# Kernel optimization log

Measured on AMD Instinct MI355X. Metric: run time of the kernel, lower is better.

Reference implementation:

```python
import jax, jax.numpy as jnp
import numpy as np
import math

C = 8  # sparsity factor c from __init__


def setup_inputs() -> dict:
    key = jax.random.key(0)
    kq, kk, kv, ki = jax.random.split(key, 4)
    B, Q, KV, D = 4, 2048, 2048, 512
    U = int(Q * math.log(KV))  # 15615 sampled keys, matches torch _sampler
    q = jax.random.normal(kq, (B, Q, D), dtype=jnp.float32)
    k = jax.random.normal(kk, (B, KV, D), dtype=jnp.float32)
    v = jax.random.normal(kv, (B, KV, D), dtype=jnp.float32)
    sample_idx = jax.random.randint(ki, (B, U), 0, KV)  # per-batch random key sample
    return {"q": q, "k": k, "v": v, "sample_idx": sample_idx}


def reference(q, k, v, sample_idx):
    B, Q, D = q.shape
    KV = k.shape[1]
    u = int(C * math.log(Q))  # number of selected queries (== 60 here)

    # _sampler: gather sampled keys per batch -> (B, U, D)
    k_bar = jnp.take_along_axis(k, sample_idx[:, :, None], axis=1)

    # sparsity measure M = max_j s_bar - mean_j s_bar, s_bar: (B, Q, U)
    s_bar = jnp.einsum('bqd,bud->bqu', q, k_bar)
    M = s_bar.max(axis=2) - s_bar.mean(axis=2)  # (B, Q)

    # top-u queries per batch
    _, top_idx = jax.lax.top_k(M, u)  # (B, u)
    q_bar = jnp.take_along_axis(q, top_idx[:, :, None], axis=1)  # (B, u, D)

    # small dense attention over full keys; NOTE: original scales by sqrt(kv_len)
    attn = jnp.einsum('bud,bkd->buk', q_bar, k) / jnp.sqrt(jnp.asarray(KV, q.dtype))
    attn = jax.nn.softmax(attn, axis=-1)
    s1 = jnp.einsum('buk,bkd->bud', attn, v)  # (B, u, D)

    # fill all positions with mean of v, then scatter attention outputs
    s = jnp.broadcast_to(v.mean(axis=1, keepdims=True), q.shape)  # (B, Q, D)
    bidx = jnp.arange(B)[:, None]
    s = s.at[bidx, top_idx].set(s1)
    return s
```

## Files before the change

### kernel.cpp

```cpp
#include <hip/hip_runtime.h>
#include <math.h>

#define BATCH 4
#define QN    2048
#define KVN   2048
#define DN    512
#define U_TOT 15615
#define NSEL  60
#define NSLOT 32
#define S1KS  64

typedef __attribute__((ext_vector_type(8))) short bf16x8;
typedef __attribute__((ext_vector_type(4))) float f32x4;

__device__ __forceinline__ unsigned short f2bf(float f) {
  unsigned u = __float_as_uint(f);
  unsigned r = (u + 0x7fffu + ((u >> 16) & 1u)) >> 16;
  return (unsigned short)r;
}
__device__ __forceinline__ float bf2f(unsigned short h) {
  return __uint_as_float(((unsigned)h) << 16);
}
__device__ __forceinline__ void gld16(const void* g, void* l) {
  __builtin_amdgcn_global_load_lds(
      (const __attribute__((address_space(1))) unsigned int*)g,
      (__attribute__((address_space(3))) unsigned int*)l, 16, 0, 0);
}

__global__ __launch_bounds__(256) void split_kernel(
    const float* __restrict__ q, const float* __restrict__ k,
    unsigned short* __restrict__ qhi, unsigned short* __restrict__ qlo,
    unsigned short* __restrict__ khi, unsigned short* __restrict__ klo)
{
  const int half = blockIdx.x >> 12;
  const int i = (blockIdx.x & 4095) * 256 + threadIdx.x;
  const float* in = half ? k : q;
  unsigned short* hi = half ? khi : qhi;
  unsigned short* lo = half ? klo : qlo;
  float4 f = reinterpret_cast<const float4*>(in)[i];
  ushort4 h, l;
  h.x = f2bf(f.x); l.x = f2bf(f.x - bf2f(h.x));
  h.y = f2bf(f.y); l.y = f2bf(f.y - bf2f(h.y));
  h.z = f2bf(f.z); l.z = f2bf(f.z - bf2f(h.z));
  h.w = f2bf(f.w); l.w = f2bf(f.w - bf2f(h.w));
  reinterpret_cast<ushort4*>(hi)[i] = h;
  reinterpret_cast<ushort4*>(lo)[i] = l;
}

__global__ __launch_bounds__(1024) void count_kernel(
    const int* __restrict__ sidx, float* __restrict__ cnt)
{
  __shared__ int h[KVN];
  const int b = blockIdx.x, t = threadIdx.x;
  for (int i = t; i < KVN; i += 1024) h[i] = 0;
  __syncthreads();
  for (int i = t; i < U_TOT; i += 1024) atomicAdd(&h[sidx[b * U_TOT + i]], 1);
  __syncthreads();
  for (int i = t; i < KVN; i += 1024) cnt[b * KVN + i] = (float)h[i];
}

#define BAR() asm volatile("s_barrier" ::: "memory")

#define PHASE_MFMA(P) \
  __builtin_amdgcn_s_setprio(1); \
  _Pragma("unroll") \
  for (int n = 0; n < 4; ++n) { \
    acc[2*(P)][n]   = __builtin_amdgcn_mfma_f32_16x16x32_bf16(a0h, bh_[n], acc[2*(P)][n], 0, 0, 0); \
    acc[2*(P)][n]   = __builtin_amdgcn_mfma_f32_16x16x32_bf16(a0h, bl_[n], acc[2*(P)][n], 0, 0, 0); \
    acc[2*(P)][n]   = __builtin_amdgcn_mfma_f32_16x16x32_bf16(a0l, bh_[n], acc[2*(P)][n], 0, 0, 0); \
    acc[2*(P)+1][n] = __builtin_amdgcn_mfma_f32_16x16x32_bf16(a1h, bh_[n], acc[2*(P)+1][n], 0, 0, 0); \
    acc[2*(P)+1][n] = __builtin_amdgcn_mfma_f32_16x16x32_bf16(a1h, bl_[n], acc[2*(P)+1][n], 0, 0, 0); \
    acc[2*(P)+1][n] = __builtin_amdgcn_mfma_f32_16x16x32_bf16(a1l, bh_[n], acc[2*(P)+1][n], 0, 0, 0); \
  } \
  __builtin_amdgcn_s_setprio(0);

#define LOAD_A(P, CB) \
  a0h = *reinterpret_cast<const bf16x8*>(&Ah[CB][(4*(P)+wr)*512 + fr8]); \
  a0l = *reinterpret_cast<const bf16x8*>(&Al[CB][(4*(P)+wr)*512 + fr8]); \
  a1h = *reinterpret_cast<const bf16x8*>(&Ah[CB][(4*(P)+2+wr)*512 + fr8]); \
  a1l = *reinterpret_cast<const bf16x8*>(&Al[CB][(4*(P)+2+wr)*512 + fr8]);

#define LOAD_B(CB) \
  _Pragma("unroll") \
  for (int n = 0; n < 4; ++n) { \
    bh_[n] = *reinterpret_cast<const bf16x8*>(&Bh[CB][wc*2048 + n*512 + fr8]); \
    bl_[n] = *reinterpret_cast<const bf16x8*>(&Bl[CB][wc*2048 + n*512 + fr8]); \
  }

#define KSTEP_MAIN(CB, NB) { \
  gld16(kh0, &Bh[NB][t*8]); gld16(kh1, &Bh[NB][4096 + t*8]); \
  gld16(kl0, &Bl[NB][t*8]); gld16(kl1, &Bl[NB][4096 + t*8]); \
  gld16(qh0, &Ah[NB][t*8]); gld16(ql0, &Al[NB][t*8]); \
  gld16(qh1, &Ah[NB][4096 + t*8]); gld16(ql1, &Al[NB][4096 + t*8]); \
  kh0 += 32; kh1 += 32; kl0 += 32; kl1 += 32; \
  qh0 += 32; qh1 += 32; ql0 += 32; ql1 += 32; \
  { \
    bf16x8 bh_[4], bl_[4], a0h, a0l, a1h, a1l; \
    LOAD_B(CB) \
    LOAD_A(0, CB) \
    PHASE_MFMA(0) \
    LOAD_A(1, CB) \
    PHASE_MFMA(1) \
    LOAD_A(2, CB) \
    PHASE_MFMA(2) \
    LOAD_A(3, CB) \
    PHASE_MFMA(3) \
  } \
  asm volatile("s_waitcnt vmcnt(0)" ::: "memory"); \
  BAR(); \
}

#define KSTEP_LAST(CB) { \
  bf16x8 bh_[4], bl_[4], a0h, a0l, a1h, a1l; \
  LOAD_B(CB) \
  LOAD_A(0, CB) \
  PHASE_MFMA(0) \
  LOAD_A(1, CB) \
  PHASE_MFMA(1) \
  LOAD_A(2, CB) \
  PHASE_MFMA(2) \
  LOAD_A(3, CB) \
  PHASE_MFMA(3) \
}

__global__ __launch_bounds__(512, 2) void s_mfma_kernel(
    const unsigned short* __restrict__ qh, const unsigned short* __restrict__ ql,
    const unsigned short* __restrict__ kh, const unsigned short* __restrict__ kl,
    const float* __restrict__ cnt, float* __restrict__ Pmax, float* __restrict__ Psum)
{
  __shared__ __align__(16) unsigned short Ah[2][8192];
  __shared__ __align__(16) unsigned short Al[2][8192];
  __shared__ __align__(16) unsigned short Bh[2][8192];
  __shared__ __align__(16) unsigned short Bl[2][8192];
  __shared__ float cnt_s[256];

  const int t = threadIdx.x;
  const int w = t >> 6;
  const int L = t & 63;
  const int lm = L & 15;
  const int wr = w >> 2;
  const int wc = w & 3;

  const int bid = blockIdx.x;
  const int xcd = bid & 7;
  const int idx = bid >> 3;
  const int b   = xcd >> 1;
  const int ji  = (xcd & 1) * 4 + (idx >> 3);
  const int qi  = idx & 7;
  const int j0  = ji * 256;
  const int q0  = qi * 256;

  if (t < 256) cnt_s[t] = cnt[b * KVN + j0 + t];

  const int srow = t >> 2;
  const int schk = (t & 3) ^ ((t >> 3) & 3);
  const int perm = (L >> 4) ^ ((lm >> 1) & 3);
  const int fr8  = (4 * lm + perm) * 8;

  const size_t kof = ((size_t)(b * KVN) + j0 + srow) * DN + (size_t)(schk * 8);
  const size_t qof = ((size_t)(b * QN) + q0 + srow) * DN + (size_t)(schk * 8);
  const unsigned short* kh0 = kh + kof;
  const unsigned short* kh1 = kh0 + (size_t)128 * DN;
  const unsigned short* kl0 = kl + kof;
  const unsigned short* kl1 = kl0 + (size_t)128 * DN;
  const unsigned short* qh0 = qh + qof;
  const unsigned short* qh1 = qh0 + (size_t)128 * DN;
  const unsigned short* ql0 = ql + qof;
  const unsigned short* ql1 = ql0 + (size_t)128 * DN;

  f32x4 acc[8][4];
#pragma unroll
  for (int m = 0; m < 8; ++m)
#pragma unroll
    for (int n = 0; n < 4; ++n) {
      acc[m][n][0] = 0.f; acc[m][n][1] = 0.f;
      acc[m][n][2] = 0.f; acc[m][n][3] = 0.f;
    }

  gld16(kh0, &Bh[0][t*8]); gld16(kh1, &Bh[0][4096 + t*8]);
  gld16(kl0, &Bl[0][t*8]); gld16(kl1, &Bl[0][4096 + t*8]);
  gld16(qh0, &Ah[0][t*8]); gld16(ql0, &Al[0][t*8]);
  gld16(qh1, &Ah[0][4096 + t*8]); gld16(ql1, &Al[0][4096 + t*8]);
  kh0 += 32; kh1 += 32; kl0 += 32; kl1 += 32;
  qh0 += 32; qh1 += 32; ql0 += 32; ql1 += 32;
  asm volatile("s_waitcnt vmcnt(0) lgkmcnt(0)" ::: "memory");
  BAR();

#pragma unroll 1
  for (int it = 0; it < 7; ++it) {
    KSTEP_MAIN(0, 1)
    KSTEP_MAIN(1, 0)
  }
  KSTEP_MAIN(0, 1)
  KSTEP_LAST(1)

  const int slot = ji * 4 + wc;
  const size_t spi = (size_t)(slot * BATCH + b);
  const int rgrp = (L >> 4) * 4;
#pragma unroll
  for (int m = 0; m < 8; ++m) {
    float mx[4] = {-INFINITY, -INFINITY, -INFINITY, -INFINITY};
    float ws[4] = {0.f, 0.f, 0.f, 0.f};
#pragma unroll
    for (int n = 0; n < 4; ++n) {
      const float cw = cnt_s[wc * 64 + n * 16 + lm];
      const bool has = (cw > 0.f);
#pragma unroll
      for (int r = 0; r < 4; ++r) {
        const float v = acc[m][n][r];
        if (has) mx[r] = fmaxf(mx[r], v);
        ws[r] = fmaf(cw, v, ws[r]);
      }
    }
#pragma unroll
    for (int r = 0; r < 4; ++r) {
      float mval = mx[r], sval = ws[r];
#pragma unroll
      for (int o = 1; o < 16; o <<= 1) {
        mval = fmaxf(mval, __shfl_xor(mval, o));
        sval += __shfl_xor(sval, o);
      }
      if (lm == 0) {
        const int qrow = q0 + (2 * m + wr) * 16 + rgrp + r;
        Pmax[spi * QN + qrow] = mval;
        Psum[spi * QN + qrow] = sval;
      }
    }
  }
}

__global__ __launch_bounds__(256) void combine_kernel(
    const float* __restrict__ Pmax, const float* __restrict__ Psum, float* __restrict__ M)
{
  const int g = blockIdx.x * 256 + threadIdx.x;
  const int b = g >> 11;
  const int qq = g & (QN - 1);
  float m = -INFINITY, s = 0.f;
#pragma unroll 4
  for (int p = 0; p < NSLOT; ++p) {
    m = fmaxf(m, Pmax[((size_t)(p * BATCH + b)) * QN + qq]);
    s += Psum[((size_t)(p * BATCH + b)) * QN + qq];
  }
  M[g] = m - s * (1.0f / (float)U_TOT);
}

__global__ __launch_bounds__(256) void select_kernel(
    const float* __restrict__ M, int* __restrict__ topidx, int* __restrict__ rowslot)
{
  const int b = blockIdx.x;
  const int t = threadIdx.x;
  unsigned long long key[8];
#pragma unroll
  for (int s = 0; s < 8; ++s) {
    const int qq = s * 256 + t;
    unsigned u = __float_as_uint(M[b * QN + qq]);
    u = (u & 0x80000000u) ? ~u : (u | 0x80000000u);
    key[s] = ((unsigned long long)u << 32) | (unsigned)(QN - qq);
    rowslot[b * QN + qq] = -1;
  }

  __shared__ unsigned hist[256];
  __shared__ unsigned long long pref_s;
  __shared__ unsigned rank_s;
  __shared__ unsigned cnt_s;
  if (t == 0) { pref_s = 0ull; rank_s = NSEL; cnt_s = 0u; }
  __syncthreads();

  for (int level = 7; level >= 0; --level) {
    const int shift = level * 8;
    hist[t] = 0;
    __syncthreads();
    const unsigned long long pref = pref_s;
    const unsigned rank = rank_s;
#pragma unroll
    for (int s = 0; s < 8; ++s) {
      const bool match = (level == 7) || ((key[s] >> (shift + 8)) == pref);
      if (match) atomicAdd(&hist[(unsigned)((key[s] >> shift) & 255u)], 1u);
    }
    __syncthreads();
    if (t < 64) {
      const unsigned h0 = hist[4 * t], h1 = hist[4 * t + 1];
      const unsigned h2 = hist[4 * t + 2], h3 = hist[4 * t + 3];
      const unsigned loc = h0 + h1 + h2 + h3;
      unsigned run = loc;
#pragma unroll
      for (int o = 1; o < 64; o <<= 1) {
        const unsigned oth = (unsigned)__shfl_down((int)run, o);
        if (t + o < 64) run += oth;
      }
      const unsigned suf = run - loc;
      const unsigned c3 = suf, c2 = c3 + h3, c1 = c2 + h2, c0 = c1 + h1;
      int hit = -1; unsigned cgt = 0;
      if      (c3 < rank && rank <= c3 + h3) { hit = 4 * t + 3; cgt = c3; }
      else if (c2 < rank && rank <= c2 + h2) { hit = 4 * t + 2; cgt = c2; }
      else if (c1 < rank && rank <= c1 + h1) { hit = 4 * t + 1; cgt = c1; }
      else if (c0 < rank && rank <= c0 + h0) { hit = 4 * t + 0; cgt = c0; }
      if (hit >= 0) {
        pref_s = ((level == 7) ? 0ull : (pref_s << 8)) | (unsigned long long)(unsigned)hit;
        rank_s = rank - cgt;
      }
    }
    __syncthreads();
  }

  const unsigned long long T = pref_s;
#pragma unroll
  for (int s = 0; s < 8; ++s) {
    if (key[s] >= T) {
      const unsigned pos = atomicAdd(&cnt_s, 1u);
      const int qsel = QN - (int)(key[s] & 0xFFFFFFFFull);
      topidx[b * 64 + pos] = qsel;
      rowslot[b * QN + qsel] = (int)pos;
    }
  }
}

#define SBM 64
#define SBN 32
#define SBK 32
__global__ __launch_bounds__(256) void scores_kernel(
    const float* __restrict__ q, const int* __restrict__ topidx,
    const float* __restrict__ k, float* __restrict__ attn)
{
  __shared__ float a_s[SBK][SBM + 4];
  __shared__ float b_s[SBK][SBN + 4];
  __shared__ int tix_s[64];
  const int t  = threadIdx.x;
  const int tx = t & 7;
  const int ty = t >> 3;
  const int kv0 = blockIdx.x * SBN;
  const int b   = blockIdx.y;
  const float* kb = k + (size_t)b * KVN * DN;

  if (t < 64) tix_s[t] = (t < NSEL) ? topidx[b * 64 + t] : 0;
  __syncthreads();

  float acc[2][4];
#pragma unroll
  for (int i = 0; i < 2; ++i)
#pragma unroll
    for (int j = 0; j < 4; ++j) acc[i][j] = 0.f;

  const int c4 = (t & 7) * 4;
  const int r0 = t >> 3;
  const int srow0 = tix_s[r0];
  const int srow1 = tix_s[r0 + 32];

  for (int d0 = 0; d0 < DN; d0 += SBK) {
#pragma unroll
    for (int rr = 0; rr < 2; ++rr) {
      int row = r0 + rr * 32;
      int srow = rr ? srow1 : srow0;
      float4 av = *reinterpret_cast<const float4*>(q + ((size_t)(b * QN) + srow) * DN + d0 + c4);
      a_s[c4 + 0][row] = av.x; a_s[c4 + 1][row] = av.y;
      a_s[c4 + 2][row] = av.z; a_s[c4 + 3][row] = av.w;
    }
    {
      float4 bv = *reinterpret_cast<const float4*>(kb + (size_t)(kv0 + r0) * DN + d0 + c4);
      b_s[c4 + 0][r0] = bv.x; b_s[c4 + 1][r0] = bv.y;
      b_s[c4 + 2][r0] = bv.z; b_s[c4 + 3][r0] = bv.w;
    }
    __syncthreads();
#pragma unroll
    for (int kk = 0; kk < SBK; ++kk) {
      const float a0 = a_s[kk][ty * 2];
      const float a1 = a_s[kk][ty * 2 + 1];
      float4 bv = *reinterpret_cast<const float4*>(&b_s[kk][tx * 4]);
      float bf[4] = {bv.x, bv.y, bv.z, bv.w};
#pragma unroll
      for (int j = 0; j < 4; ++j) {
        acc[0][j] = fmaf(a0, bf[j], acc[0][j]);
        acc[1][j] = fmaf(a1, bf[j], acc[1][j]);
      }
    }
    __syncthreads();
  }

#pragma unroll
  for (int i = 0; i < 2; ++i) {
    int j = ty * 2 + i;
    if (j < NSEL) {
      float4 o = make_float4(acc[i][0], acc[i][1], acc[i][2], acc[i][3]);
      *reinterpret_cast<float4*>(attn + ((size_t)(b * NSEL + j)) * KVN + kv0 + tx * 4) = o;
    }
  }
}

__global__ __launch_bounds__(256) void softmax_kernel(float* __restrict__ attn)
{
  __shared__ float buf[KVN];
  __shared__ float red[256];
  const int t = threadIdx.x;
  float* row = attn + (size_t)blockIdx.x * KVN;

  float m = -INFINITY;
  for (int i = t; i < KVN; i += 256) { float v = row[i]; buf[i] = v; m = fmaxf(m, v); }
  red[t] = m;
  __syncthreads();
  for (int off = 128; off > 0; off >>= 1) {
    if (t < off) red[t] = fmaxf(red[t], red[t + off]);
    __syncthreads();
  }
  m = red[0];
  __syncthreads();

  const float sc = 0.022097086912079608f;
  float s = 0.f;
  for (int i = t; i < KVN; i += 256) { float e = __expf((buf[i] - m) * sc); buf[i] = e; s += e; }
  red[t] = s;
  __syncthreads();
  for (int off = 128; off > 0; off >>= 1) {
    if (t < off) red[t] += red[t + off];
    __syncthreads();
  }
  float inv = 1.f / red[0];
  for (int i = t; i < KVN; i += 256) row[i] = buf[i] * inv;
}

__global__ __launch_bounds__(256) void s1_partial_kernel(
    const float* __restrict__ attn, const float* __restrict__ v,
    float* __restrict__ part, float* __restrict__ vpart)
{
  __shared__ float a_s[32][61];
  const int t    = threadIdx.x;
  const int dv4  = t & 63;
  const int jg   = t >> 6;
  const int dh   = blockIdx.x;
  const int b    = blockIdx.y;
  const int ks   = blockIdx.z;
  const int kv0  = ks * 32;
  const int dbase = dh * 256 + dv4 * 4;

  for (int x = t; x < NSEL * 32; x += 256) {
    const int j = x >> 5, kk = x & 31;
    a_s[kk][j] = attn[((size_t)(b * NSEL + j)) * KVN + kv0 + kk];
  }
  __syncthreads();

  f32x4 acc[15];
#pragma unroll
  for (int i = 0; i < 15; ++i) { acc[i][0] = 0.f; acc[i][1] = 0.f; acc[i][2] = 0.f; acc[i][3] = 0.f; }
  f32x4 vsum; vsum[0] = 0.f; vsum[1] = 0.f; vsum[2] = 0.f; vsum[3] = 0.f;

  const float* vb = v + ((size_t)b * KVN + kv0) * DN + dbase;
#pragma unroll 8
  for (int kk = 0; kk < 32; ++kk) {
    const f32x4 vv = *reinterpret_cast<const f32x4*>(vb + (size_t)kk * DN);
    if (jg == 0) { vsum[0] += vv[0]; vsum[1] += vv[1]; vsum[2] += vv[2]; vsum[3] += vv[3]; }
#pragma unroll
    for (int jj = 0; jj < 15; ++jj) {
      const float a = a_s[kk][jg * 15 + jj];
      acc[jj][0] = fmaf(a, vv[0], acc[jj][0]);
      acc[jj][1] = fmaf(a, vv[1], acc[jj][1]);
      acc[jj][2] = fmaf(a, vv[2], acc[jj][2]);
      acc[jj][3] = fmaf(a, vv[3], acc[jj][3]);
    }
  }

#pragma unroll
  for (int jj = 0; jj < 15; ++jj) {
    const int j = jg * 15 + jj;
    *reinterpret_cast<f32x4*>(
        part + ((size_t)((ks * BATCH + b) * NSEL) + j) * DN + dbase) = acc[jj];
  }
  if (jg == 0)
    *reinterpret_cast<f32x4*>(vpart + ((size_t)(ks * BATCH + b)) * DN + dbase) = vsum;
}

__global__ void vmean_combine_kernel(const float* __restrict__ vpart, float* __restrict__ vmean)
{
  int idx = blockIdx.x * 256 + threadIdx.x;
  if (idx < BATCH * DN) {
    int b = idx / DN, d = idx % DN;
    float s = 0.f;
    for (int c = 0; c < S1KS; ++c) s += vpart[(size_t)(c * BATCH + b) * DN + d];
    vmean[idx] = s * (1.0f / (float)KVN);
  }
}

__global__ __launch_bounds__(256) void out_kernel(
    const float* __restrict__ part, const float* __restrict__ vmean,
    const int* __restrict__ rowslot, float* __restrict__ out)
{
  const int gid = blockIdx.x * 256 + threadIdx.x;
  const int d4 = gid & 127;
  const int qq = (gid >> 7) & (QN - 1);
  const int b  = gid >> 18;
  const int slot = rowslot[b * QN + qq];
  f32x4 o;
  if (slot >= 0) {
    o[0] = 0.f; o[1] = 0.f; o[2] = 0.f; o[3] = 0.f;
    for (int ks = 0; ks < S1KS; ++ks) {
      const f32x4 p = reinterpret_cast<const f32x4*>(part)[
          ((size_t)((ks * BATCH + b) * NSEL) + slot) * (DN / 4) + d4];
      o[0] += p[0]; o[1] += p[1]; o[2] += p[2]; o[3] += p[3];
    }
  } else {
    o = reinterpret_cast<const f32x4*>(vmean)[b * (DN / 4) + d4];
  }
  reinterpret_cast<f32x4*>(out)[gid] = o;
}

extern "C" void kernel_launch(void* const* d_in, const int* in_sizes, int n_in,
                              void* d_out, int out_size, void* d_ws, size_t ws_size,
                              hipStream_t stream) {
  const float* q    = (const float*)d_in[0];
  const float* k    = (const float*)d_in[1];
  const float* v    = (const float*)d_in[2];
  const int*   sidx = (const int*)d_in[3];
  float* out = (float*)d_out;
  char*  W   = (char*)d_ws;

  const size_t NEL = (size_t)BATCH * QN * DN;
  unsigned short* qh = (unsigned short*)W;
  unsigned short* ql = qh + NEL;
  unsigned short* kh = ql + NEL;
  unsigned short* kl = kh + NEL;

  char* W2 = W + 37748736;
  float* cnt     = (float*)W2;
  float* Pmax    = (float*)(W2 + 32768);
  float* Psum    = (float*)(W2 + 32768 + 1048576);
  float* Mbuf    = (float*)(W2 + 32768 + 2097152);
  int*   topidx  = (int*)(W2 + 32768 + 2097152 + 32768);
  int*   rowslot = (int*)(W2 + 32768 + 2097152 + 32768 + 4096);

  float* attn  = (float*)W;
  float* part  = (float*)(W + 2097152);
  float* vpart = (float*)(W + 33554432);
  float* vmean = (float*)(W + 34078720);

  split_kernel<<<dim3(8192), 256, 0, stream>>>(q, k, qh, ql, kh, kl);
  count_kernel<<<dim3(BATCH), 1024, 0, stream>>>(sidx, cnt);
  s_mfma_kernel<<<dim3(256), 512, 0, stream>>>(qh, ql, kh, kl, cnt, Pmax, Psum);
  combine_kernel<<<dim3(BATCH * QN / 256), 256, 0, stream>>>(Pmax, Psum, Mbuf);
  select_kernel<<<dim3(BATCH), 256, 0, stream>>>(Mbuf, topidx, rowslot);
  scores_kernel<<<dim3(KVN / SBN, BATCH), 256, 0, stream>>>(q, topidx, k, attn);
  softmax_kernel<<<dim3(BATCH * NSEL), 256, 0, stream>>>(attn);
  s1_partial_kernel<<<dim3(2, BATCH, S1KS), 256, 0, stream>>>(attn, v, part, vpart);
  vmean_combine_kernel<<<dim3(8), 256, 0, stream>>>(vpart, vmean);
  out_kernel<<<dim3(4096), 256, 0, stream>>>(part, vmean, rowslot, out);
}
```

Before: 220.8 us.

## Fuse preprocessing, combine, and softmax into neighboring kernels with deferred normalization

Merges the bf16 split, sample count histogram, and v column-sum into one launch, folds the M combine step into the top-k selection kernel, and removes the separate softmax kernel. Exp is now applied in the scores epilogue, with row sums accumulated in s1_partial and division applied in out_kernel. The s1 KV chunk doubles to halve partial sums. This cuts launch count and attn round trips, but drops max-subtraction in softmax, which risks overflow for large scores, and uses float atomics for the v mean.

Measured after the change: 238.6 us. 1.08x slower.

```diff
diff --git a/kernel.cpp b/kernel.cpp
--- a/kernel.cpp
+++ b/kernel.cpp
@@ -8,7 +8,7 @@
 #define U_TOT 15615
 #define NSEL  60
 #define NSLOT 32
-#define S1KS  64
+#define S1KS  32
 
 typedef __attribute__((ext_vector_type(8))) short bf16x8;
 typedef __attribute__((ext_vector_type(4))) float f32x4;
@@ -27,36 +27,50 @@
       (__attribute__((address_space(3))) unsigned int*)l, 16, 0, 0);
 }
 
-__global__ __launch_bounds__(256) void split_kernel(
+__global__ __launch_bounds__(256) void pre_kernel(
     const float* __restrict__ q, const float* __restrict__ k,
+    const float* __restrict__ v, const int* __restrict__ sidx,
     unsigned short* __restrict__ qhi, unsigned short* __restrict__ qlo,
-    unsigned short* __restrict__ khi, unsigned short* __restrict__ klo)
-{
-  const int half = blockIdx.x >> 12;
-  const int i = (blockIdx.x & 4095) * 256 + threadIdx.x;
-  const float* in = half ? k : q;
-  unsigned short* hi = half ? khi : qhi;
-  unsigned short* lo = half ? klo : qlo;
-  float4 f = reinterpret_cast<const float4*>(in)[i];
-  ushort4 h, l;
-  h.x = f2bf(f.x); l.x = f2bf(f.x - bf2f(h.x));
-  h.y = f2bf(f.y); l.y = f2bf(f.y - bf2f(h.y));
-  h.z = f2bf(f.z); l.z = f2bf(f.z - bf2f(h.z));
-  h.w = f2bf(f.w); l.w = f2bf(f.w - bf2f(h.w));
-  reinterpret_cast<ushort4*>(hi)[i] = h;
-  reinterpret_cast<ushort4*>(lo)[i] = l;
-}
-
-__global__ __launch_bounds__(1024) void count_kernel(
-    const int* __restrict__ sidx, float* __restrict__ cnt)
+    unsigned short* __restrict__ khi, unsigned short* __restrict__ klo,
+    float* __restrict__ cnt, float* __restrict__ vmean_raw)
 {
   __shared__ int h[KVN];
-  const int b = blockIdx.x, t = threadIdx.x;
-  for (int i = t; i < KVN; i += 1024) h[i] = 0;
-  __syncthreads();
-  for (int i = t; i < U_TOT; i += 1024) atomicAdd(&h[sidx[b * U_TOT + i]], 1);
-  __syncthreads();
-  for (int i = t; i < KVN; i += 1024) cnt[b * KVN + i] = (float)h[i];
+  const int bid = blockIdx.x;
+  const int t = threadIdx.x;
+
+  if (bid < 8192) {
+    const int half = bid >> 12;
+    const int i = (bid & 4095) * 256 + t;
+    const float* in = half ? k : q;
+    unsigned short* hi = half ? khi : qhi;
+    unsigned short* lo = half ? klo : qlo;
+    float4 f = reinterpret_cast<const float4*>(in)[i];
+    ushort4 hh, ll;
+    hh.x = f2bf(f.x); ll.x = f2bf(f.x - bf2f(hh.x));
+    hh.y = f2bf(f.y); ll.y = f2bf(f.y - bf2f(hh.y));
+    hh.z = f2bf(f.z); ll.z = f2bf(f.z - bf2f(hh.z));
+    hh.w = f2bf(f.w); ll.w = f2bf(f.w - bf2f(hh.w));
+    reinterpret_cast<ushort4*>(hi)[i] = hh;
+    reinterpret_cast<ushort4*>(lo)[i] = ll;
+  } else if (bid < 8196) {
+    const int b = bid - 8192;
+    for (int i = t; i < KVN; i += 256) h[i] = 0;
+    __syncthreads();
+    for (int i = t; i < U_TOT; i += 256) atomicAdd(&h[sidx[b * U_TOT + i]], 1);
+    __syncthreads();
+    for (int i = t; i < KVN; i += 256) cnt[b * KVN + i] = (float)h[i];
+  } else {
+    const int idx = bid - 8196;
+    const int b = idx >> 4, ch = idx & 15;
+    const float* vb = v + ((size_t)(b * KVN) + ch * 128) * DN;
+    float s0 = 0.f, s1 = 0.f;
+    for (int r = 0; r < 128; ++r) {
+      s0 += vb[(size_t)r * DN + t];
+      s1 += vb[(size_t)r * DN + t + 256];
+    }
+    atomicAdd(&vmean_raw[b * DN + t], s0);
+    atomicAdd(&vmean_raw[b * DN + t + 256], s1);
+  }
 }
 
 #define BAR() asm volatile("s_barrier" ::: "memory")
@@ -229,23 +243,9 @@
   }
 }
 
-__global__ __launch_bounds__(256) void combine_kernel(
-    const float* __restrict__ Pmax, const float* __restrict__ Psum, float* __restrict__ M)
-{
-  const int g = blockIdx.x * 256 + threadIdx.x;
-  const int b = g >> 11;
-  const int qq = g & (QN - 1);
-  float m = -INFINITY, s = 0.f;
-#pragma unroll 4
-  for (int p = 0; p < NSLOT; ++p) {
-    m = fmaxf(m, Pmax[((size_t)(p * BATCH + b)) * QN + qq]);
-    s += Psum[((size_t)(p * BATCH + b)) * QN + qq];
-  }
-  M[g] = m - s * (1.0f / (float)U_TOT);
-}
-
 __global__ __launch_bounds__(256) void select_kernel(
-    const float* __restrict__ M, int* __restrict__ topidx, int* __restrict__ rowslot)
+    const float* __restrict__ Pmax, const float* __restrict__ Psum,
+    int* __restrict__ topidx, int* __restrict__ rowslot)
 {
   const int b = blockIdx.x;
   const int t = threadIdx.x;
@@ -253,7 +253,14 @@
 #pragma unroll
   for (int s = 0; s < 8; ++s) {
     const int qq = s * 256 + t;
-    unsigned u = __float_as_uint(M[b * QN + qq]);
+    float m = -INFINITY, sm = 0.f;
+#pragma unroll 4
+    for (int p = 0; p < NSLOT; ++p) {
+      m = fmaxf(m, Pmax[((size_t)(p * BATCH + b)) * QN + qq]);
+      sm += Psum[((size_t)(p * BATCH + b)) * QN + qq];
+    }
+    const float Mv = m - sm * (1.0f / (float)U_TOT);
+    unsigned u = __float_as_uint(Mv);
     u = (u & 0x80000000u) ? ~u : (u | 0x80000000u);
     key[s] = ((unsigned long long)u << 32) | (unsigned)(QN - qq);
     rowslot[b * QN + qq] = -1;
@@ -376,77 +383,52 @@
     __syncthreads();
   }
 
+  const float sc = 0.022097086912079608f;
 #pragma unroll
   for (int i = 0; i < 2; ++i) {
     int j = ty * 2 + i;
     if (j < NSEL) {
-      float4 o = make_float4(acc[i][0], acc[i][1], acc[i][2], acc[i][3]);
+      float4 o = make_float4(__expf(acc[i][0] * sc), __expf(acc[i][1] * sc),
+                             __expf(acc[i][2] * sc), __expf(acc[i][3] * sc));
       *reinterpret_cast<float4*>(attn + ((size_t)(b * NSEL + j)) * KVN + kv0 + tx * 4) = o;
     }
   }
-}
-
-__global__ __launch_bounds__(256) void softmax_kernel(float* __restrict__ attn)
-{
-  __shared__ float buf[KVN];
-  __shared__ float red[256];
-  const int t = threadIdx.x;
-  float* row = attn + (size_t)blockIdx.x * KVN;
-
-  float m = -INFINITY;
-  for (int i = t; i < KVN; i += 256) { float v = row[i]; buf[i] = v; m = fmaxf(m, v); }
-  red[t] = m;
-  __syncthreads();
-  for (int off = 128; off > 0; off >>= 1) {
-    if (t < off) red[t] = fmaxf(red[t], red[t + off]);
-    __syncthreads();
-  }
-  m = red[0];
-  __syncthreads();
-
-  const float sc = 0.022097086912079608f;
-  float s = 0.f;
-  for (int i = t; i < KVN; i += 256) { float e = __expf((buf[i] - m) * sc); buf[i] = e; s += e; }
-  red[t] = s;
-  __syncthreads();
-  for (int off = 128; off > 0; off >>= 1) {
-    if (t < off) red[t] += red[t + off];
-    __syncthreads();
-  }
-  float inv = 1.f / red[0];
-  for (int i = t; i < KVN; i += 256) row[i] = buf[i] * inv;
 }
 
 __global__ __launch_bounds__(256) void s1_partial_kernel(
     const float* __restrict__ attn, const float* __restrict__ v,
-    float* __restrict__ part, float* __restrict__ vpart)
+    float* __restrict__ part, float* __restrict__ epart)
 {
-  __shared__ float a_s[32][61];
+  __shared__ float a_s[64][61];
   const int t    = threadIdx.x;
   const int dv4  = t & 63;
   const int jg   = t >> 6;
   const int dh   = blockIdx.x;
   const int b    = blockIdx.y;
   const int ks   = blockIdx.z;
-  const int kv0  = ks * 32;
+  const int kv0  = ks * 64;
   const int dbase = dh * 256 + dv4 * 4;
 
-  for (int x = t; x < NSEL * 32; x += 256) {
-    const int j = x >> 5, kk = x & 31;
+  for (int x = t; x < NSEL * 64; x += 256) {
+    const int j = x >> 6, kk = x & 63;
     a_s[kk][j] = attn[((size_t)(b * NSEL + j)) * KVN + kv0 + kk];
   }
   __syncthreads();
 
+  if (dh == 0 && t < NSEL) {
+    float es = 0.f;
+    for (int kk = 0; kk < 64; ++kk) es += a_s[kk][t];
+    epart[(ks * BATCH + b) * 64 + t] = es;
+  }
+
   f32x4 acc[15];
 #pragma unroll
   for (int i = 0; i < 15; ++i) { acc[i][0] = 0.f; acc[i][1] = 0.f; acc[i][2] = 0.f; acc[i][3] = 0.f; }
-  f32x4 vsum; vsum[0] = 0.f; vsum[1] = 0.f; vsum[2] = 0.f; vsum[3] = 0.f;
 
   const float* vb = v + ((size_t)b * KVN + kv0) * DN + dbase;
-#pragma unroll 8
-  for (int kk = 0; kk < 32; ++kk) {
+#pragma unroll 4
+  for (int kk = 0; kk < 64; ++kk) {
     const f32x4 vv = *reinterpret_cast<const f32x4*>(vb + (size_t)kk * DN);
-    if (jg == 0) { vsum[0] += vv[0]; vsum[1] += vv[1]; vsum[2] += vv[2]; vsum[3] += vv[3]; }
 #pragma unroll
     for (int jj = 0; jj < 15; ++jj) {
       const float a = a_s[kk][jg * 15 + jj];
@@ -463,24 +445,12 @@
     *reinterpret_cast<f32x4*>(
         part + ((size_t)((ks * BATCH + b) * NSEL) + j) * DN + dbase) = acc[jj];
   }
-  if (jg == 0)
-    *reinterpret_cast<f32x4*>(vpart + ((size_t)(ks * BATCH + b)) * DN + dbase) = vsum;
-}
-
-__global__ void vmean_combine_kernel(const float* __restrict__ vpart, float* __restrict__ vmean)
-{
-  int idx = blockIdx.x * 256 + threadIdx.x;
-  if (idx < BATCH * DN) {
-    int b = idx / DN, d = idx % DN;
-    float s = 0.f;
-    for (int c = 0; c < S1KS; ++c) s += vpart[(size_t)(c * BATCH + b) * DN + d];
-    vmean[idx] = s * (1.0f / (float)KVN);
-  }
 }
 
 __global__ __launch_bounds__(256) void out_kernel(
-    const float* __restrict__ part, const float* __restrict__ vmean,
-    const int* __restrict__ rowslot, float* __restrict__ out)
+    const float* __restrict__ part, const float* __restrict__ epart,
+    const float* __restrict__ vmean_raw, const int* __restrict__ rowslot,
+    float* __restrict__ out)
 {
   const int gid = blockIdx.x * 256 + threadIdx.x;
   const int d4 = gid & 127;
@@ -490,13 +460,19 @@
   f32x4 o;
   if (slot >= 0) {
     o[0] = 0.f; o[1] = 0.f; o[2] = 0.f; o[3] = 0.f;
+    float es = 0.f;
     for (int ks = 0; ks < S1KS; ++ks) {
       const f32x4 p = reinterpret_cast<const f32x4*>(part)[
           ((size_t)((ks * BATCH + b) * NSEL) + slot) * (DN / 4) + d4];
       o[0] += p[0]; o[1] += p[1]; o[2] += p[2]; o[3] += p[3];
-    }
+      es += epart[(ks * BATCH + b) * 64 + slot];
+    }
+    const float inv = 1.f / es;
+    o[0] *= inv; o[1] *= inv; o[2] *= inv; o[3] *= inv;
   } else {
-    o = reinterpret_cast<const f32x4*>(vmean)[b * (DN / 4) + d4];
+    o = reinterpret_cast<const f32x4*>(vmean_raw)[b * (DN / 4) + d4];
+    const float s = 1.0f / (float)KVN;
+    o[0] *= s; o[1] *= s; o[2] *= s; o[3] *= s;
   }
   reinterpret_cast<f32x4*>(out)[gid] = o;
 }
@@ -521,23 +497,19 @@
   float* cnt     = (float*)W2;
   float* Pmax    = (float*)(W2 + 32768);
   float* Psum    = (float*)(W2 + 32768 + 1048576);
-  float* Mbuf    = (float*)(W2 + 32768 + 2097152);
   int*   topidx  = (int*)(W2 + 32768 + 2097152 + 32768);
   int*   rowslot = (int*)(W2 + 32768 + 2097152 + 32768 + 4096);
 
   float* attn  = (float*)W;
   float* part  = (float*)(W + 2097152);
-  float* vpart = (float*)(W + 33554432);
+  float* epart = (float*)(W + 33554432);
   float* vmean = (float*)(W + 34078720);
 
-  split_kernel<<<dim3(8192), 256, 0, stream>>>(q, k, qh, ql, kh, kl);
-  count_kernel<<<dim3(BATCH), 1024, 0, stream>>>(sidx, cnt);
+  hipMemsetAsync(vmean, 0, BATCH * DN * sizeof(float), stream);
+  pre_kernel<<<dim3(8260), 256, 0, stream>>>(q, k, v, sidx, qh, ql, kh, kl, cnt, vmean);
   s_mfma_kernel<<<dim3(256), 512, 0, stream>>>(qh, ql, kh, kl, cnt, Pmax, Psum);
-  combine_kernel<<<dim3(BATCH * QN / 256), 256, 0, stream>>>(Pmax, Psum, Mbuf);
-  select_kernel<<<dim3(BATCH), 256, 0, stream>>>(Mbuf, topidx, rowslot);
+  select_kernel<<<dim3(BATCH), 256, 0, stream>>>(Pmax, Psum, topidx, rowslot);
   scores_kernel<<<dim3(KVN / SBN, BATCH), 256, 0, stream>>>(q, topidx, k, attn);
-  softmax_kernel<<<dim3(BATCH * NSEL), 256, 0, stream>>>(attn);
-  s1_partial_kernel<<<dim3(2, BATCH, S1KS), 256, 0, stream>>>(attn, v, part, vpart);
-  vmean_combine_kernel<<<dim3(8), 256, 0, stream>>>(vpart, vmean);
-  out_kernel<<<dim3(4096), 256, 0, stream>>>(part, vmean, rowslot, out);
-}
+  s1_partial_kernel<<<dim3(2, BATCH, S1KS), 256, 0, stream>>>(attn, v, part, epart);
+  out_kernel<<<dim3(4096), 256, 0, stream>>>(part, epart, vmean, rowslot, out);
+}
```
